# Optimization experiments

Hardware: AMD Instinct MI355X
Metric: run time of the kernel (lower is better)

Reference implementation:

```python
import jax, jax.numpy as jnp
import numpy as np

B, S, D, H = 64, 512, 256, 512

def setup_inputs() -> dict:
    key = jax.random.key(0)
    ks = jax.random.split(key, 16)
    s_in = 1.0 / np.sqrt(D)
    s_h = 1.0 / np.sqrt(H)
    inp = {
        "inputs": jax.random.normal(ks[0], (B, S, D), jnp.float32),
        # input-side gate weights (stored [D,H], equiv to torch Linear weight.T)
        "Wf": jax.random.uniform(ks[1], (D, H), jnp.float32, -s_in, s_in),
        "Wi": jax.random.uniform(ks[2], (D, H), jnp.float32, -s_in, s_in),
        "Wo": jax.random.uniform(ks[3], (D, H), jnp.float32, -s_in, s_in),
        "Wc": jax.random.uniform(ks[4], (D, H), jnp.float32, -s_in, s_in),
        "bf": jax.random.uniform(ks[5], (H,), jnp.float32, -s_in, s_in),
        "bi": jax.random.uniform(ks[6], (H,), jnp.float32, -s_in, s_in),
        "bo": jax.random.uniform(ks[7], (H,), jnp.float32, -s_in, s_in),
        "bc": jax.random.uniform(ks[8], (H,), jnp.float32, -s_in, s_in),
        # recurrent weights (bias=False)
        "Uf": jax.random.uniform(ks[9], (H, H), jnp.float32, -s_h, s_h),
        "Ui": jax.random.uniform(ks[10], (H, H), jnp.float32, -s_h, s_h),
        "Uo": jax.random.uniform(ks[11], (H, H), jnp.float32, -s_h, s_h),
        "Uc": jax.random.uniform(ks[12], (H, H), jnp.float32, -s_h, s_h),
        # output head
        "Wfc": jax.random.uniform(ks[13], (H, 1), jnp.float32, -s_h, s_h),
        "bfc": jax.random.uniform(ks[14], (1,), jnp.float32, -s_h, s_h),
    }
    return inp


def reference(inputs, Wf, Wi, Wo, Wc, bf, bi, bo, bc, Uf, Ui, Uo, Uc, Wfc, bfc):
    # Precompute all input-side gate projections in one big GEMM: [B,S,4H]
    Wx = jnp.concatenate([Wf, Wi, Wo, Wc], axis=1)            # [D,4H]
    bx = jnp.concatenate([bf, bi, bo, bc], axis=0)            # [4H]
    gx = jnp.einsum('bsd,dg->bsg', inputs, Wx) + bx           # [B,S,4H]
    Uh = jnp.concatenate([Uf, Ui, Uo, Uc], axis=1)            # [H,4H]

    h0 = jnp.zeros((inputs.shape[0], Uf.shape[0]), inputs.dtype)
    c0 = jnp.zeros_like(h0)
    Hd = Uf.shape[0]

    def step(carry, gx_t):
        h, c = carry
        g = gx_t + h @ Uh                                     # [B,4H]
        f_t = jax.nn.sigmoid(g[:, 0 * Hd:1 * Hd])
        i_t = jax.nn.sigmoid(g[:, 1 * Hd:2 * Hd])
        o_t = jax.nn.sigmoid(g[:, 2 * Hd:3 * Hd])
        chat = jnp.tanh(g[:, 3 * Hd:4 * Hd])
        c = f_t * c + i_t * chat
        h = o_t * jnp.tanh(c)
        return (h, c), h

    (h_t, c_t), hs = jax.lax.scan(step, (h0, c0), jnp.swapaxes(gx, 0, 1))
    outputs = jnp.swapaxes(hs, 0, 1)                          # [B,S,H]
    predictions = jnp.einsum('bsh,ho->bso', outputs, Wfc) + bfc
    return predictions, h_t, c_t
```

## Files before the change

kernel.cpp:

```cpp
#include <hip/hip_runtime.h>
#include <hip/hip_bf16.h>

#define B_ 64
#define S_ 512
#define D_ 256
#define H_ 512

typedef __attribute__((ext_vector_type(8))) short bf16x8;
typedef __attribute__((ext_vector_type(4))) float f32x4;
typedef __attribute__((ext_vector_type(4))) unsigned int uint4v;
typedef unsigned short ushort_t;

__device__ __forceinline__ ushort_t f2bf(float f) {
    __hip_bfloat16 h = __float2bfloat16(f);
    return *reinterpret_cast<ushort_t*>(&h);
}
__device__ __forceinline__ float sigmoid_f(float x) { return 1.f / (1.f + __expf(-x)); }
__device__ __forceinline__ float tanh_f(float x) { return 1.f - 2.f / (__expf(2.f * x) + 1.f); }

__device__ __forceinline__ void lds_barrier() {
    asm volatile("s_waitcnt lgkmcnt(0)\n\ts_barrier" ::: "memory");
}

__global__ __launch_bounds__(512, 2) void lstm_rec(
    const float* __restrict__ X,
    const float* __restrict__ Wf, const float* __restrict__ Wi,
    const float* __restrict__ Wo, const float* __restrict__ Wc,
    const float* __restrict__ bfp, const float* __restrict__ bip,
    const float* __restrict__ bop, const float* __restrict__ bcp,
    const float* __restrict__ Uf, const float* __restrict__ Ui,
    const float* __restrict__ Uo, const float* __restrict__ Uc,
    const float* __restrict__ Wfc,
    float* __restrict__ pred, unsigned int* __restrict__ hbufU,
    unsigned int* __restrict__ flags,
    float* __restrict__ outH, float* __restrict__ outC)
{
    __shared__ ushort_t hS[16 * 520];
    __shared__ ushort_t xS[16 * 264];
    __shared__ float gact[4][16][68];

    const int tid  = threadIdx.x;
    const int w    = tid >> 6;
    const int lane = tid & 63;
    const int q    = lane >> 4;
    const int m    = lane & 15;
    const int gate = w >> 1;
    const int half = w & 1;
    const int g    = blockIdx.x & 3;
    const int s    = blockIdx.x >> 2;

    const int ncol0 = s * 64 + half * 32 + m;
    const int ncol1 = ncol0 + 16;

    const float* Ug = (gate == 0) ? Uf : (gate == 1) ? Ui : (gate == 2) ? Uo : Uc;
    const float* Wg = (gate == 0) ? Wf : (gate == 1) ? Wi : (gate == 2) ? Wo : Wc;
    const float* bg = (gate == 0) ? bfp : (gate == 1) ? bip : (gate == 2) ? bop : bcp;

    const float bias0 = bg[ncol0];
    const float bias1 = bg[ncol1];

    bf16x8 UF[2][16];
    bf16x8 WF[2][8];
    #pragma unroll
    for (int tt = 0; tt < 2; ++tt) {
        const int nc = tt ? ncol1 : ncol0;
        #pragma unroll
        for (int ks = 0; ks < 16; ++ks) {
            bf16x8 v;
            #pragma unroll
            for (int j = 0; j < 8; ++j)
                v[j] = (short)f2bf(Ug[(ks * 32 + q * 8 + j) * H_ + nc]);
            UF[tt][ks] = v;
        }
        #pragma unroll
        for (int ks = 0; ks < 8; ++ks) {
            bf16x8 v;
            #pragma unroll
            for (int j = 0; j < 8; ++j)
                v[j] = (short)f2bf(Wg[(ks * 32 + q * 8 + j) * H_ + nc]);
            WF[tt][ks] = v;
        }
    }

    const int urow  = tid >> 5;
    const int upair = tid & 31;
    const float2 wfc2 = *(const float2*)&Wfc[s * 64 + 2 * upair];

    float cr0 = 0.f, cr1 = 0.f;

    unsigned int* flagsG = flags + g * 64;
    const int myflag = s * 8 + w;

    {
        const float* xsrc = &X[((size_t)(g * 16 + urow) * S_ + 0) * D_ + upair * 8];
        float4 a = *(const float4*)xsrc;
        float4 b = *(const float4*)(xsrc + 4);
        bf16x8 v;
        v[0] = (short)f2bf(a.x); v[1] = (short)f2bf(a.y);
        v[2] = (short)f2bf(a.z); v[3] = (short)f2bf(a.w);
        v[4] = (short)f2bf(b.x); v[5] = (short)f2bf(b.y);
        v[6] = (short)f2bf(b.z); v[7] = (short)f2bf(b.w);
        *(bf16x8*)&xS[urow * 264 + upair * 8] = v;
    }

    float4 xr0, xr1;

    for (int t = 0; t < S_; ++t) {
        if (t > 0) {
            const unsigned int tgt = (unsigned int)t;
            for (;;) {
                unsigned int f = __hip_atomic_load(&flagsG[lane],
                                                   __ATOMIC_RELAXED, __HIP_MEMORY_SCOPE_AGENT);
                if (__ballot(f >= tgt) == ~0ull) break;
                __builtin_amdgcn_s_sleep(1);
            }
        }

        {
            const int row  = tid >> 5;
            const int dcol = (tid & 31) * 8;
            const unsigned int* p0 = &hbufU[(size_t)((t % 3) * B_ + g * 16 + row) * 256 + dcol];
            const unsigned int* p1 = p0 + 4;
            uint4v ra, rb;
            asm volatile(
                "global_load_dwordx4 %0, %2, off sc0 sc1\n\t"
                "global_load_dwordx4 %1, %3, off sc0 sc1\n\t"
                "s_waitcnt vmcnt(0)"
                : "=v"(ra), "=v"(rb) : "v"(p0), "v"(p1) : "memory");
            *(uint4v*)&hS[row * 520 + dcol * 2]     = ra;
            *(uint4v*)&hS[row * 520 + dcol * 2 + 8] = rb;
        }
        lds_barrier();

        if (t + 1 < S_) {
            const float* xsrc = &X[((size_t)(g * 16 + urow) * S_ + (t + 1)) * D_ + upair * 8];
            xr0 = *(const float4*)xsrc;
            xr1 = *(const float4*)(xsrc + 4);
        }
        f32x4 accA0 = {bias0, bias0, bias0, bias0};
        f32x4 accA1 = {bias1, bias1, bias1, bias1};
        f32x4 accB0 = {0.f, 0.f, 0.f, 0.f};
        f32x4 accB1 = {0.f, 0.f, 0.f, 0.f};
        #pragma unroll
        for (int ks = 0; ks < 8; ++ks) {
            bf16x8 a = *(const bf16x8*)&xS[m * 264 + ks * 32 + q * 8];
            accA0 = __builtin_amdgcn_mfma_f32_16x16x32_bf16(a, WF[0][ks], accA0, 0, 0, 0);
            accA1 = __builtin_amdgcn_mfma_f32_16x16x32_bf16(a, WF[1][ks], accA1, 0, 0, 0);
        }
        #pragma unroll
        for (int ks = 0; ks < 16; ++ks) {
            bf16x8 a = *(const bf16x8*)&hS[m * 520 + ks * 32 + q * 8];
            accB0 = __builtin_amdgcn_mfma_f32_16x16x32_bf16(a, UF[0][ks], accB0, 0, 0, 0);
            accB1 = __builtin_amdgcn_mfma_f32_16x16x32_bf16(a, UF[1][ks], accB1, 0, 0, 0);
        }
        #pragma unroll
        for (int j = 0; j < 4; ++j) {
            float v0 = accA0[j] + accB0[j];
            float v1 = accA1[j] + accB1[j];
            v0 = (gate < 3) ? sigmoid_f(v0) : tanh_f(v0);
            v1 = (gate < 3) ? sigmoid_f(v1) : tanh_f(v1);
            gact[gate][q * 4 + j][half * 32 + m]      = v0;
            gact[gate][q * 4 + j][half * 32 + 16 + m] = v1;
        }
        lds_barrier();

        float2 f2v = *(const float2*)&gact[0][urow][2 * upair];
        float2 i2v = *(const float2*)&gact[1][urow][2 * upair];
        float2 o2v = *(const float2*)&gact[2][urow][2 * upair];
        float2 ch2 = *(const float2*)&gact[3][urow][2 * upair];
        cr0 = f2v.x * cr0 + i2v.x * ch2.x;
        cr1 = f2v.y * cr1 + i2v.y * ch2.y;
        float hv0 = o2v.x * tanh_f(cr0);
        float hv1 = o2v.y * tanh_f(cr1);

        float pv = hv0 * wfc2.x + hv1 * wfc2.y;

        if (t < S_ - 1) {
            unsigned int packed = (unsigned int)f2bf(hv0) | ((unsigned int)f2bf(hv1) << 16);
            __hip_atomic_store(
                &hbufU[(size_t)(((t + 1) % 3) * B_ + g * 16 + urow) * 256 + s * 32 + upair],
                packed, __ATOMIC_RELAXED, __HIP_MEMORY_SCOPE_AGENT);
            asm volatile("s_waitcnt vmcnt(0)" ::: "memory");
            if (lane == 0) {
                __hip_atomic_store(&flagsG[myflag], (unsigned int)(t + 1),
                                   __ATOMIC_RELAXED, __HIP_MEMORY_SCOPE_AGENT);
            }
            bf16x8 v;
            v[0] = (short)f2bf(xr0.x); v[1] = (short)f2bf(xr0.y);
            v[2] = (short)f2bf(xr0.z); v[3] = (short)f2bf(xr0.w);
            v[4] = (short)f2bf(xr1.x); v[5] = (short)f2bf(xr1.y);
            v[6] = (short)f2bf(xr1.z); v[7] = (short)f2bf(xr1.w);
            *(bf16x8*)&xS[urow * 264 + upair * 8] = v;
        } else {
            *(float2*)&outH[(g * 16 + urow) * H_ + s * 64 + 2 * upair] = make_float2(hv0, hv1);
            *(float2*)&outC[(g * 16 + urow) * H_ + s * 64 + 2 * upair] = make_float2(cr0, cr1);
        }

        pv += __shfl_xor(pv, 16);
        pv += __shfl_xor(pv, 8);
        pv += __shfl_xor(pv, 4);
        pv += __shfl_xor(pv, 2);
        pv += __shfl_xor(pv, 1);
        if (upair == 0) atomicAdd(&pred[(g * 16 + urow) * S_ + t], pv);
    }
}

__global__ void pred_fin(const float* __restrict__ pred,
                         const float* __restrict__ bfc,
                         float* __restrict__ out)
{
    int i = blockIdx.x * blockDim.x + threadIdx.x;
    if (i < B_ * S_) out[i] = pred[i] + bfc[0];
}

extern "C" void kernel_launch(void* const* d_in, const int* in_sizes, int n_in,
                              void* d_out, int out_size, void* d_ws, size_t ws_size,
                              hipStream_t stream) {
    const float* X   = (const float*)d_in[0];
    const float* Wf  = (const float*)d_in[1];
    const float* Wi  = (const float*)d_in[2];
    const float* Wo  = (const float*)d_in[3];
    const float* Wc  = (const float*)d_in[4];
    const float* bfp = (const float*)d_in[5];
    const float* bip = (const float*)d_in[6];
    const float* bop = (const float*)d_in[7];
    const float* bcp = (const float*)d_in[8];
    const float* Uf  = (const float*)d_in[9];
    const float* Ui  = (const float*)d_in[10];
    const float* Uo  = (const float*)d_in[11];
    const float* Uc  = (const float*)d_in[12];
    const float* Wfc = (const float*)d_in[13];
    const float* bfc = (const float*)d_in[14];

    float*        pred  = (float*)d_ws;
    unsigned int* hbufU = (unsigned int*)((char*)d_ws + 131072);
    unsigned int* flags = (unsigned int*)((char*)d_ws + 131072 + 196608);

    hipMemsetAsync(d_ws, 0, 131072 + 196608 + 2048, stream);

    float* out = (float*)d_out;
    lstm_rec<<<32, 512, 0, stream>>>(X, Wf, Wi, Wo, Wc, bfp, bip, bop, bcp,
                                     Uf, Ui, Uo, Uc, Wfc,
                                     pred, hbufU, flags,
                                     out + 32768, out + 65536);
    pred_fin<<<128, 256, 0, stream>>>(pred, bfc, out);
}
```

Before: 2.425 ms.

## Group recurrent blocks by XCD and use L2-scoped sync when groups are co-located

The kernel now launches 64 blocks. Each block reads its hardware XCD id and publishes it to a table, then the blocks rank themselves so that the first 32 form four groups of eight, ideally all on one XCD; the surplus blocks exit. When a group sits on a single XCD, flag polling uses an atomic-add-of-zero, and the h-buffer exchange uses sc0-only loads and stores, keeping traffic in the shared L2 instead of going through system-coherent memory. Flags are padded to 128 bytes apart to avoid false sharing. The risks are the extra startup rendezvous and the correctness of XCD-local coherence, and groups that cannot be placed on one XCD fall back to the old path.

```diff
diff --git a/kernel.cpp b/kernel.cpp
--- a/kernel.cpp
+++ b/kernel.cpp
@@ -32,12 +32,13 @@
     const float* __restrict__ Uo, const float* __restrict__ Uc,
     const float* __restrict__ Wfc,
     float* __restrict__ pred, unsigned int* __restrict__ hbufU,
-    unsigned int* __restrict__ flags,
+    unsigned int* __restrict__ flags, unsigned int* __restrict__ xcdtab,
     float* __restrict__ outH, float* __restrict__ outC)
 {
     __shared__ ushort_t hS[16 * 520];
     __shared__ ushort_t xS[16 * 264];
     __shared__ float gact[4][16][68];
+    __shared__ int meta[2];
 
     const int tid  = threadIdx.x;
     const int w    = tid >> 6;
@@ -46,8 +47,36 @@
     const int m    = lane & 15;
     const int gate = w >> 1;
     const int half = w & 1;
-    const int g    = blockIdx.x & 3;
-    const int s    = blockIdx.x >> 2;
+
+    if (w == 0) {
+        unsigned int xcd;
+        asm volatile("s_getreg_b32 %0, hwreg(HW_REG_XCC_ID)" : "=s"(xcd));
+        xcd &= 15u;
+        if (lane == 0)
+            __hip_atomic_store(&xcdtab[blockIdx.x], xcd + 1u,
+                               __ATOMIC_RELEASE, __HIP_MEMORY_SCOPE_AGENT);
+        unsigned int entry;
+        for (;;) {
+            entry = __hip_atomic_load(&xcdtab[lane], __ATOMIC_ACQUIRE, __HIP_MEMORY_SCOPE_AGENT);
+            if (__ballot(entry != 0u) == ~0ull) break;
+            __builtin_amdgcn_s_sleep(1);
+        }
+        const unsigned int xcd_j = entry - 1u;
+        const unsigned int key_j = (xcd_j << 8) | (unsigned int)lane;
+        const unsigned int mykey = (xcd << 8) | (unsigned int)blockIdx.x;
+        const int rank = __popcll(__ballot(key_j < mykey));
+        const int c_lt = __popcll(__ballot(xcd_j < xcd));
+        const int c_eq = __popcll(__ballot(xcd_j == xcd));
+        const int gg   = rank >> 3;
+        const bool uni = (c_lt <= gg * 8) && (gg * 8 + 8 <= c_lt + c_eq);
+        if (lane == 0) { meta[0] = rank; meta[1] = uni ? 1 : 0; }
+    }
+    __syncthreads();
+    const int  rank    = meta[0];
+    const bool uniform = meta[1] != 0;
+    if (rank >= 32) return;
+    const int g = rank >> 3;
+    const int s = rank & 7;
 
     const int ncol0 = s * 64 + half * 32 + m;
     const int ncol1 = ncol0 + 16;
@@ -88,7 +117,7 @@
 
     float cr0 = 0.f, cr1 = 0.f;
 
-    unsigned int* flagsG = flags + g * 64;
+    unsigned int* flagsG = flags + (size_t)g * 64 * 32;
     const int myflag = s * 8 + w;
 
     {
@@ -108,11 +137,25 @@
     for (int t = 0; t < S_; ++t) {
         if (t > 0) {
             const unsigned int tgt = (unsigned int)t;
-            for (;;) {
-                unsigned int f = __hip_atomic_load(&flagsG[lane],
-                                                   __ATOMIC_RELAXED, __HIP_MEMORY_SCOPE_AGENT);
-                if (__ballot(f >= tgt) == ~0ull) break;
-                __builtin_amdgcn_s_sleep(1);
+            unsigned int* fp = &flagsG[lane * 32];
+            if (uniform) {
+                for (;;) {
+                    unsigned int f;
+                    asm volatile(
+                        "global_atomic_add %0, %1, %2, off sc0\n\ts_waitcnt vmcnt(0)"
+                        : "=v"(f) : "v"(fp), "v"(0u) : "memory");
+                    if (__ballot(f >= tgt) == ~0ull) break;
+                    __builtin_amdgcn_s_sleep(1);
+                }
+            } else {
+                for (;;) {
+                    unsigned int f;
+                    asm volatile(
+                        "global_load_dword %0, %1, off sc0 sc1\n\ts_waitcnt vmcnt(0)"
+                        : "=v"(f) : "v"(fp) : "memory");
+                    if (__ballot(f >= tgt) == ~0ull) break;
+                    __builtin_amdgcn_s_sleep(1);
+                }
             }
         }
 
@@ -122,11 +165,19 @@
             const unsigned int* p0 = &hbufU[(size_t)((t % 3) * B_ + g * 16 + row) * 256 + dcol];
             const unsigned int* p1 = p0 + 4;
             uint4v ra, rb;
-            asm volatile(
-                "global_load_dwordx4 %0, %2, off sc0 sc1\n\t"
-                "global_load_dwordx4 %1, %3, off sc0 sc1\n\t"
-                "s_waitcnt vmcnt(0)"
-                : "=v"(ra), "=v"(rb) : "v"(p0), "v"(p1) : "memory");
+            if (uniform) {
+                asm volatile(
+                    "global_load_dwordx4 %0, %2, off sc0\n\t"
+                    "global_load_dwordx4 %1, %3, off sc0\n\t"
+                    "s_waitcnt vmcnt(0)"
+                    : "=v"(ra), "=v"(rb) : "v"(p0), "v"(p1) : "memory");
+            } else {
+                asm volatile(
+                    "global_load_dwordx4 %0, %2, off sc0 sc1\n\t"
+                    "global_load_dwordx4 %1, %3, off sc0 sc1\n\t"
+                    "s_waitcnt vmcnt(0)"
+                    : "=v"(ra), "=v"(rb) : "v"(p0), "v"(p1) : "memory");
+            }
             *(uint4v*)&hS[row * 520 + dcol * 2]     = ra;
             *(uint4v*)&hS[row * 520 + dcol * 2 + 8] = rb;
         }
@@ -177,13 +228,22 @@
 
         if (t < S_ - 1) {
             unsigned int packed = (unsigned int)f2bf(hv0) | ((unsigned int)f2bf(hv1) << 16);
-            __hip_atomic_store(
-                &hbufU[(size_t)(((t + 1) % 3) * B_ + g * 16 + urow) * 256 + s * 32 + upair],
-                packed, __ATOMIC_RELAXED, __HIP_MEMORY_SCOPE_AGENT);
-            asm volatile("s_waitcnt vmcnt(0)" ::: "memory");
-            if (lane == 0) {
-                __hip_atomic_store(&flagsG[myflag], (unsigned int)(t + 1),
-                                   __ATOMIC_RELAXED, __HIP_MEMORY_SCOPE_AGENT);
+            unsigned int* hdst =
+                &hbufU[(size_t)(((t + 1) % 3) * B_ + g * 16 + urow) * 256 + s * 32 + upair];
+            unsigned int* fdst = &flagsG[myflag * 32];
+            unsigned int fval  = (unsigned int)(t + 1);
+            if (uniform) {
+                asm volatile("global_store_dword %0, %1, off sc0" :: "v"(hdst), "v"(packed) : "memory");
+                asm volatile("s_waitcnt vmcnt(0)" ::: "memory");
+                if (lane == 0) {
+                    asm volatile("global_atomic_swap %0, %1, off" :: "v"(fdst), "v"(fval) : "memory");
+                }
+            } else {
+                asm volatile("global_store_dword %0, %1, off sc0 sc1" :: "v"(hdst), "v"(packed) : "memory");
+                asm volatile("s_waitcnt vmcnt(0)" ::: "memory");
+                if (lane == 0) {
+                    asm volatile("global_atomic_swap %0, %1, off sc1" :: "v"(fdst), "v"(fval) : "memory");
+                }
             }
             bf16x8 v;
             v[0] = (short)f2bf(xr0.x); v[1] = (short)f2bf(xr0.y);
@@ -232,16 +292,17 @@
     const float* Wfc = (const float*)d_in[13];
     const float* bfc = (const float*)d_in[14];
 
-    float*        pred  = (float*)d_ws;
-    unsigned int* hbufU = (unsigned int*)((char*)d_ws + 131072);
-    unsigned int* flags = (unsigned int*)((char*)d_ws + 131072 + 196608);
-
-    hipMemsetAsync(d_ws, 0, 131072 + 196608 + 2048, stream);
+    float*        pred   = (float*)d_ws;
+    unsigned int* hbufU  = (unsigned int*)((char*)d_ws + 131072);
+    unsigned int* flags  = (unsigned int*)((char*)d_ws + 327680);
+    unsigned int* xcdtab = (unsigned int*)((char*)d_ws + 360448);
+
+    hipMemsetAsync(d_ws, 0, 360448 + 256, stream);
 
     float* out = (float*)d_out;
-    lstm_rec<<<32, 512, 0, stream>>>(X, Wf, Wi, Wo, Wc, bfp, bip, bop, bcp,
+    lstm_rec<<<64, 512, 0, stream>>>(X, Wf, Wi, Wo, Wc, bfp, bip, bop, bcp,
                                      Uf, Ui, Uo, Uc, Wfc,
-                                     pred, hbufU, flags,
+                                     pred, hbufU, flags, xcdtab,
                                      out + 32768, out + 65536);
     pred_fin<<<128, 256, 0, stream>>>(pred, bfc, out);
 }
```

Result: slower. 2.592 ms (+6.9%).

## Tag hidden-state words with step number instead of separate flag polling

Applied to the files above, without the earlier changes.

Each bf16 hidden value is now stored in its own 32-bit word with the timestep in the upper half. Consumers spin on the data itself rather than on per-wave flags, which removes the store-then-wait and flag-store round trip on every recurrent step. The prediction head also writes per-slice partial sums into a separate buffer that the final kernel reduces, replacing atomicAdd. In exchange, the hidden-state buffer doubles in size and each thread polls 16 words per step.

```diff
diff --git a/kernel.cpp b/kernel.cpp
--- a/kernel.cpp
+++ b/kernel.cpp
@@ -31,8 +31,7 @@
     const float* __restrict__ Uf, const float* __restrict__ Ui,
     const float* __restrict__ Uo, const float* __restrict__ Uc,
     const float* __restrict__ Wfc,
-    float* __restrict__ pred, unsigned int* __restrict__ hbufU,
-    unsigned int* __restrict__ flags,
+    float* __restrict__ predP, unsigned int* __restrict__ hbufT,
     float* __restrict__ outH, float* __restrict__ outC)
 {
     __shared__ ushort_t hS[16 * 520];
@@ -87,9 +86,6 @@
     const float2 wfc2 = *(const float2*)&Wfc[s * 64 + 2 * upair];
 
     float cr0 = 0.f, cr1 = 0.f;
-
-    unsigned int* flagsG = flags + g * 64;
-    const int myflag = s * 8 + w;
 
     {
         const float* xsrc = &X[((size_t)(g * 16 + urow) * S_ + 0) * D_ + upair * 8];
@@ -106,37 +102,39 @@
     float4 xr0, xr1;
 
     for (int t = 0; t < S_; ++t) {
-        if (t > 0) {
-            const unsigned int tgt = (unsigned int)t;
-            for (;;) {
-                unsigned int f = __hip_atomic_load(&flagsG[lane],
-                                                   __ATOMIC_RELAXED, __HIP_MEMORY_SCOPE_AGENT);
-                if (__ballot(f >= tgt) == ~0ull) break;
-                __builtin_amdgcn_s_sleep(1);
-            }
-        }
-
-        {
-            const int row  = tid >> 5;
-            const int dcol = (tid & 31) * 8;
-            const unsigned int* p0 = &hbufU[(size_t)((t % 3) * B_ + g * 16 + row) * 256 + dcol];
-            const unsigned int* p1 = p0 + 4;
-            uint4v ra, rb;
-            asm volatile(
-                "global_load_dwordx4 %0, %2, off sc0 sc1\n\t"
-                "global_load_dwordx4 %1, %3, off sc0 sc1\n\t"
-                "s_waitcnt vmcnt(0)"
-                : "=v"(ra), "=v"(rb) : "v"(p0), "v"(p1) : "memory");
-            *(uint4v*)&hS[row * 520 + dcol * 2]     = ra;
-            *(uint4v*)&hS[row * 520 + dcol * 2 + 8] = rb;
-        }
-        lds_barrier();
-
         if (t + 1 < S_) {
             const float* xsrc = &X[((size_t)(g * 16 + urow) * S_ + (t + 1)) * D_ + upair * 8];
             xr0 = *(const float4*)xsrc;
             xr1 = *(const float4*)(xsrc + 4);
         }
+
+        {
+            const unsigned int tgt = (unsigned int)t;
+            const unsigned int* hb =
+                hbufT + (size_t)((t % 3) * B_ + g * 16 + urow) * 512 + upair * 16;
+            unsigned int v[16];
+            for (;;) {
+                #pragma unroll
+                for (int i = 0; i < 16; ++i)
+                    v[i] = __hip_atomic_load(&hb[i], __ATOMIC_RELAXED, __HIP_MEMORY_SCOPE_AGENT);
+                bool ok = true;
+                #pragma unroll
+                for (int i = 0; i < 16; ++i) ok &= ((v[i] >> 16) >= tgt);
+                if (ok) break;
+                __builtin_amdgcn_s_sleep(1);
+            }
+            uint4v pa, pb;
+            #pragma unroll
+            for (int i = 0; i < 4; ++i)
+                pa[i] = (v[2 * i] & 0xffffu) | (v[2 * i + 1] << 16);
+            #pragma unroll
+            for (int i = 0; i < 4; ++i)
+                pb[i] = (v[8 + 2 * i] & 0xffffu) | (v[8 + 2 * i + 1] << 16);
+            *(uint4v*)&hS[urow * 520 + upair * 16]     = pa;
+            *(uint4v*)&hS[urow * 520 + upair * 16 + 8] = pb;
+        }
+        lds_barrier();
+
         f32x4 accA0 = {bias0, bias0, bias0, bias0};
         f32x4 accA1 = {bias1, bias1, bias1, bias1};
         f32x4 accB0 = {0.f, 0.f, 0.f, 0.f};
@@ -176,15 +174,14 @@
         float pv = hv0 * wfc2.x + hv1 * wfc2.y;
 
         if (t < S_ - 1) {
-            unsigned int packed = (unsigned int)f2bf(hv0) | ((unsigned int)f2bf(hv1) << 16);
-            __hip_atomic_store(
-                &hbufU[(size_t)(((t + 1) % 3) * B_ + g * 16 + urow) * 256 + s * 32 + upair],
-                packed, __ATOMIC_RELAXED, __HIP_MEMORY_SCOPE_AGENT);
-            asm volatile("s_waitcnt vmcnt(0)" ::: "memory");
-            if (lane == 0) {
-                __hip_atomic_store(&flagsG[myflag], (unsigned int)(t + 1),
-                                   __ATOMIC_RELAXED, __HIP_MEMORY_SCOPE_AGENT);
-            }
+            const unsigned int tagv = (unsigned int)(t + 1) << 16;
+            unsigned int* hdst =
+                hbufT + (size_t)(((t + 1) % 3) * B_ + g * 16 + urow) * 512 + s * 64 + 2 * upair;
+            __hip_atomic_store(&hdst[0], tagv | (unsigned int)f2bf(hv0),
+                               __ATOMIC_RELAXED, __HIP_MEMORY_SCOPE_AGENT);
+            __hip_atomic_store(&hdst[1], tagv | (unsigned int)f2bf(hv1),
+                               __ATOMIC_RELAXED, __HIP_MEMORY_SCOPE_AGENT);
+
             bf16x8 v;
             v[0] = (short)f2bf(xr0.x); v[1] = (short)f2bf(xr0.y);
             v[2] = (short)f2bf(xr0.z); v[3] = (short)f2bf(xr0.w);
@@ -201,16 +198,23 @@
         pv += __shfl_xor(pv, 4);
         pv += __shfl_xor(pv, 2);
         pv += __shfl_xor(pv, 1);
-        if (upair == 0) atomicAdd(&pred[(g * 16 + urow) * S_ + t], pv);
-    }
-}
-
-__global__ void pred_fin(const float* __restrict__ pred,
+        if (upair == 0)
+            predP[((size_t)s * B_ + g * 16 + urow) * S_ + t] = pv;
+    }
+}
+
+__global__ void pred_fin(const float* __restrict__ predP,
                          const float* __restrict__ bfc,
                          float* __restrict__ out)
 {
     int i = blockIdx.x * blockDim.x + threadIdx.x;
-    if (i < B_ * S_) out[i] = pred[i] + bfc[0];
+    if (i < B_ * S_) {
+        float v = bfc[0];
+        #pragma unroll
+        for (int s = 0; s < 8; ++s)
+            v += predP[(size_t)s * B_ * S_ + i];
+        out[i] = v;
+    }
 }
 
 extern "C" void kernel_launch(void* const* d_in, const int* in_sizes, int n_in,
@@ -232,16 +236,15 @@
     const float* Wfc = (const float*)d_in[13];
     const float* bfc = (const float*)d_in[14];
 
-    float*        pred  = (float*)d_ws;
-    unsigned int* hbufU = (unsigned int*)((char*)d_ws + 131072);
-    unsigned int* flags = (unsigned int*)((char*)d_ws + 131072 + 196608);
-
-    hipMemsetAsync(d_ws, 0, 131072 + 196608 + 2048, stream);
+    unsigned int* hbufT = (unsigned int*)d_ws;
+    float*        predP = (float*)((char*)d_ws + 393216);
+
+    hipMemsetAsync(d_ws, 0, 393216, stream);
 
     float* out = (float*)d_out;
     lstm_rec<<<32, 512, 0, stream>>>(X, Wf, Wi, Wo, Wc, bfp, bip, bop, bcp,
                                      Uf, Ui, Uo, Uc, Wfc,
-                                     pred, hbufU, flags,
+                                     predP, hbufT,
                                      out + 32768, out + 65536);
-    pred_fin<<<128, 256, 0, stream>>>(pred, bfc, out);
-}
+    pred_fin<<<128, 256, 0, stream>>>(predP, bfc, out);
+}
```

New measurement: 3.461 ms. +42.7%, slower.
